# Optimization experiments

Measured on AMD Instinct MI355X. Metric: run time of the kernel, lower is better.

Reference implementation:

```python
import jax, jax.numpy as jnp
import numpy as np


def setup_inputs() -> dict:
    key = jax.random.key(0)
    kq, kk, kv = jax.random.split(key, 3)
    shape = (2, 8, 1024, 64)  # [B, H, L, D]
    return {
        "q": jax.random.normal(kq, shape, dtype=jnp.float32),
        "k": jax.random.normal(kk, shape, dtype=jnp.float32),
        "v": jax.random.normal(kv, shape, dtype=jnp.float32),
    }


def reference(q, k, v):
    B, H, L, D = q.shape
    eps = 1e-6
    q = jax.nn.relu(q).reshape(B * H, L, D)
    k = jax.nn.relu(k).reshape(B * H, L, D)
    v = jax.nn.relu(v).reshape(B * H, L, D)

    # cosFormer positional reweighting: pi/2 * (i+1)/L
    idx = (jnp.pi / 2) * jnp.arange(1, L + 1, dtype=q.dtype) / L  # [L]
    s = jnp.sin(idx)[None, :, None]  # [1, L, 1]
    c = jnp.cos(idx)[None, :, None]

    q_ = jnp.concatenate([q * s, q * c], axis=-1)  # [N, L, 2D]
    k_ = jnp.concatenate([k * s, k * c], axis=-1)  # [N, L, 2D]

    # causal linear attention via cumulative kv outer product
    kv = jnp.einsum("nld,nlm->nldm", k_, v)        # [N, L, 2D, D]
    kv_cum = jnp.cumsum(kv, axis=1)                  # [N, L, 2D, D]
    qkv = jnp.einsum("nld,nldm->nlm", q_, kv_cum)  # [N, L, D]

    k_cum = jnp.cumsum(k_, axis=1)                   # [N, L, 2D]
    denom = jnp.clip(jnp.einsum("nld,nld->nl", q_, k_cum), eps, None)

    out = qkv / denom[..., None]
    return out.reshape(B, H, L, D)
```

## Files before the change

### kernel.cpp

```cpp
#include <hip/hip_runtime.h>

#define N_HEADS 16
#define L_SEQ   1024
#define D_HEAD  64
#define D2      128
#define T_CHUNK 32
#define N_CHUNK (L_SEQ / T_CHUNK)
#define KV_ELEMS (D2 * D_HEAD)

#define ROWP 140
#define PARTP 132

__device__ __forceinline__ int pad_col(int d2) { return d2 + 4 * (d2 >> 5); }

#define SINCOS_SCALE 1.53398078788564122971e-3f

__device__ __forceinline__ float red8_dpp(float x) {
    x += __int_as_float(__builtin_amdgcn_mov_dpp(__float_as_int(x), 0xB1, 0xF, 0xF, true));
    x += __int_as_float(__builtin_amdgcn_mov_dpp(__float_as_int(x), 0x4E, 0xF, 0xF, true));
    x += __int_as_float(__builtin_amdgcn_mov_dpp(__float_as_int(x), 0x141, 0xF, 0xF, true));
    return x;
}

__global__ __launch_bounds__(256, 2) void k1_chunk_sums(
    const float* __restrict__ k, const float* __restrict__ v,
    float* __restrict__ sumkv, float* __restrict__ sumk)
{
    __shared__ __attribute__((aligned(16))) float k_s[T_CHUNK][ROWP];
    __shared__ __attribute__((aligned(16))) float v_s[T_CHUNK][D_HEAD];
    __shared__ float s_tab[T_CHUNK], c_tab[T_CHUNK];

    const int c = blockIdx.x, n = blockIdx.y;
    const int tid = threadIdx.x;
    const int base = (n * L_SEQ + c * T_CHUNK) * D_HEAD;

    if (tid < T_CHUNK) {
        float th = SINCOS_SCALE * (float)(c * T_CHUNK + tid + 1);
        s_tab[tid] = __sinf(th);
        c_tab[tid] = __cosf(th);
    }
    __syncthreads();

    const float4* k4g = (const float4*)(k + base);
    const float4* v4g = (const float4*)(v + base);
#pragma unroll
    for (int j = 0; j < 2; ++j) {
        int i4 = j * 256 + tid;
        int l = i4 >> 4, d = (i4 & 15) << 2;
        float4 kk = k4g[i4], vv = v4g[i4];
        kk.x = fmaxf(kk.x, 0.f); kk.y = fmaxf(kk.y, 0.f);
        kk.z = fmaxf(kk.z, 0.f); kk.w = fmaxf(kk.w, 0.f);
        vv.x = fmaxf(vv.x, 0.f); vv.y = fmaxf(vv.y, 0.f);
        vv.z = fmaxf(vv.z, 0.f); vv.w = fmaxf(vv.w, 0.f);
        float s = s_tab[l], cs = c_tab[l];
        *(float4*)&k_s[l][pad_col(d)]      = make_float4(kk.x*s,  kk.y*s,  kk.z*s,  kk.w*s);
        *(float4*)&k_s[l][pad_col(d + 64)] = make_float4(kk.x*cs, kk.y*cs, kk.z*cs, kk.w*cs);
        *(float4*)&v_s[l][d] = vv;
    }
    __syncthreads();

    if (tid < D2) {
        int pc = pad_col(tid);
        float ks = 0.f;
#pragma unroll
        for (int l = 0; l < T_CHUNK; ++l) ks += k_s[l][pc];
        sumk[(n * N_CHUNK + c) * D2 + tid] = ks;
    }

    const int g = tid & 7, mh = (tid >> 3) << 1;
    const int gbase = pad_col(16 * g);

    float st0[16], st1[16];
#pragma unroll
    for (int j = 0; j < 16; ++j) { st0[j] = 0.f; st1[j] = 0.f; }

    for (int l = 0; l < T_CHUNK; ++l) {
        float2 vm = *(const float2*)&v_s[l][mh];
        const float4* kv4 = (const float4*)&k_s[l][gbase];
#pragma unroll
        for (int jj = 0; jj < 4; ++jj) {
            float4 kk = kv4[jj];
            st0[4*jj+0] = fmaf(kk.x, vm.x, st0[4*jj+0]);
            st1[4*jj+0] = fmaf(kk.x, vm.y, st1[4*jj+0]);
            st0[4*jj+1] = fmaf(kk.y, vm.x, st0[4*jj+1]);
            st1[4*jj+1] = fmaf(kk.y, vm.y, st1[4*jj+1]);
            st0[4*jj+2] = fmaf(kk.z, vm.x, st0[4*jj+2]);
            st1[4*jj+2] = fmaf(kk.z, vm.y, st1[4*jj+2]);
            st0[4*jj+3] = fmaf(kk.w, vm.x, st0[4*jj+3]);
            st1[4*jj+3] = fmaf(kk.w, vm.y, st1[4*jj+3]);
        }
    }

    float4* dst = (float4*)(sumkv + (size_t)(n * N_CHUNK + c) * KV_ELEMS);
#pragma unroll
    for (int j4 = 0; j4 < 4; ++j4) {
        dst[(2*j4+0)*256 + tid] = make_float4(st0[4*j4], st0[4*j4+1], st0[4*j4+2], st0[4*j4+3]);
        dst[(2*j4+1)*256 + tid] = make_float4(st1[4*j4], st1[4*j4+1], st1[4*j4+2], st1[4*j4+3]);
    }
}

__global__ __launch_bounds__(256) void k2_prefix(
    float* __restrict__ sumkv, float* __restrict__ sumk)
{
    const int x = blockIdx.x, n = blockIdx.y;
    const int tid = threadIdx.x;

    if (x < 32) {
        float* base = sumkv + (size_t)n * N_CHUNK * KV_ELEMS + x * 256 + tid;
        float t[N_CHUNK];
#pragma unroll
        for (int c = 0; c < N_CHUNK; ++c) t[c] = base[c * KV_ELEMS];
        float r = 0.f;
#pragma unroll
        for (int c = 0; c < N_CHUNK; ++c) { base[c * KV_ELEMS] = r; r += t[c]; }
    } else if (tid < D2) {
        float* bk = sumk + n * N_CHUNK * D2 + tid;
        float t[N_CHUNK];
#pragma unroll
        for (int c = 0; c < N_CHUNK; ++c) t[c] = bk[c * D2];
        float r = 0.f;
#pragma unroll
        for (int c = 0; c < N_CHUNK; ++c) { bk[c * D2] = r; r += t[c]; }
    }
}

__global__ __launch_bounds__(256, 2) void k3_output(
    const float* __restrict__ q, const float* __restrict__ k,
    const float* __restrict__ v, const float* __restrict__ sumkv,
    const float* __restrict__ sumk, float* __restrict__ out)
{
    __shared__ __attribute__((aligned(16))) float k_s[T_CHUNK][ROWP];
    __shared__ __attribute__((aligned(16))) float q_s[T_CHUNK][ROWP];
    __shared__ __attribute__((aligned(16))) float v_s[T_CHUNK][D_HEAD];
    __shared__ __attribute__((aligned(16))) float part_s[T_CHUNK][PARTP];
    __shared__ float rden_s[T_CHUNK];
    __shared__ __attribute__((aligned(16))) float out_s[T_CHUNK][D_HEAD];
    __shared__ float s_tab[T_CHUNK], c_tab[T_CHUNK];

    const int c = blockIdx.x, n = blockIdx.y;
    const int tid = threadIdx.x;
    const int base = (n * L_SEQ + c * T_CHUNK) * D_HEAD;

    if (tid < T_CHUNK) {
        float th = SINCOS_SCALE * (float)(c * T_CHUNK + tid + 1);
        s_tab[tid] = __sinf(th);
        c_tab[tid] = __cosf(th);
    }
    __syncthreads();

    const float4* q4g = (const float4*)(q + base);
    const float4* k4g = (const float4*)(k + base);
    const float4* v4g = (const float4*)(v + base);
#pragma unroll
    for (int j = 0; j < 2; ++j) {
        int i4 = j * 256 + tid;
        int l = i4 >> 4, d = (i4 & 15) << 2;
        float4 kk = k4g[i4], qq = q4g[i4], vv = v4g[i4];
        kk.x = fmaxf(kk.x, 0.f); kk.y = fmaxf(kk.y, 0.f);
        kk.z = fmaxf(kk.z, 0.f); kk.w = fmaxf(kk.w, 0.f);
        qq.x = fmaxf(qq.x, 0.f); qq.y = fmaxf(qq.y, 0.f);
        qq.z = fmaxf(qq.z, 0.f); qq.w = fmaxf(qq.w, 0.f);
        vv.x = fmaxf(vv.x, 0.f); vv.y = fmaxf(vv.y, 0.f);
        vv.z = fmaxf(vv.z, 0.f); vv.w = fmaxf(vv.w, 0.f);
        float s = s_tab[l], cs = c_tab[l];
        *(float4*)&k_s[l][pad_col(d)]      = make_float4(kk.x*s,  kk.y*s,  kk.z*s,  kk.w*s);
        *(float4*)&k_s[l][pad_col(d + 64)] = make_float4(kk.x*cs, kk.y*cs, kk.z*cs, kk.w*cs);
        *(float4*)&q_s[l][pad_col(d)]      = make_float4(qq.x*s,  qq.y*s,  qq.z*s,  qq.w*s);
        *(float4*)&q_s[l][pad_col(d + 64)] = make_float4(qq.x*cs, qq.y*cs, qq.z*cs, qq.w*cs);
        *(float4*)&v_s[l][d] = vv;
    }

    const float4* pkv = (const float4*)(sumkv + (size_t)(n * N_CHUNK + c) * KV_ELEMS);
    float4 s0 = pkv[0*256 + tid];
    float4 s1 = pkv[1*256 + tid];
    float4 s2 = pkv[2*256 + tid];
    float4 s3 = pkv[3*256 + tid];
    float4 s4 = pkv[4*256 + tid];
    float4 s5 = pkv[5*256 + tid];
    float4 s6 = pkv[6*256 + tid];
    float4 s7 = pkv[7*256 + tid];
    float kc = 0.f;
    if (tid < D2) kc = sumk[(n * N_CHUNK + c) * D2 + tid];

    __syncthreads();

    if (tid < D2) {
        int pc = pad_col(tid);
#pragma unroll
        for (int l = 0; l < T_CHUNK; ++l) {
            kc += k_s[l][pc];
            part_s[l][tid] = q_s[l][pc] * kc;
        }
    }
    __syncthreads();

    {
        int l = tid >> 3, j = tid & 7;
        const float4* p4 = (const float4*)&part_s[l][j * 16];
        float4 aa = p4[0], bb = p4[1], cc = p4[2], dd = p4[3];
        float sum = ((aa.x + aa.y) + (aa.z + aa.w)) + ((bb.x + bb.y) + (bb.z + bb.w))
                  + ((cc.x + cc.y) + (cc.z + cc.w)) + ((dd.x + dd.y) + (dd.z + dd.w));
        sum = red8_dpp(sum);
        if (j == 0) rden_s[l] = 1.f / fmaxf(sum, 1e-6f);
    }
    __syncthreads();

    const int g = tid & 7, mh = (tid >> 3) << 1;
    const int gbase = pad_col(16 * g);

    float st0[16], st1[16];
    st0[0]=s0.x;  st0[1]=s0.y;  st0[2]=s0.z;  st0[3]=s0.w;
    st1[0]=s1.x;  st1[1]=s1.y;  st1[2]=s1.z;  st1[3]=s1.w;
    st0[4]=s2.x;  st0[5]=s2.y;  st0[6]=s2.z;  st0[7]=s2.w;
    st1[4]=s3.x;  st1[5]=s3.y;  st1[6]=s3.z;  st1[7]=s3.w;
    st0[8]=s4.x;  st0[9]=s4.y;  st0[10]=s4.z; st0[11]=s4.w;
    st1[8]=s5.x;  st1[9]=s5.y;  st1[10]=s5.z; st1[11]=s5.w;
    st0[12]=s6.x; st0[13]=s6.y; st0[14]=s6.z; st0[15]=s6.w;
    st1[12]=s7.x; st1[13]=s7.y; st1[14]=s7.z; st1[15]=s7.w;

    for (int l = 0; l < T_CHUNK; ++l) {
        float2 vm = *(const float2*)&v_s[l][mh];
        const float4* kv4 = (const float4*)&k_s[l][gbase];
        const float4* qv4 = (const float4*)&q_s[l][gbase];
        float a0 = 0.f, a1 = 0.f;
#pragma unroll
        for (int jj = 0; jj < 4; ++jj) {
            float4 kk = kv4[jj];
            float4 qq = qv4[jj];
            st0[4*jj+0] = fmaf(kk.x, vm.x, st0[4*jj+0]); a0 = fmaf(qq.x, st0[4*jj+0], a0);
            st1[4*jj+0] = fmaf(kk.x, vm.y, st1[4*jj+0]); a1 = fmaf(qq.x, st1[4*jj+0], a1);
            st0[4*jj+1] = fmaf(kk.y, vm.x, st0[4*jj+1]); a0 = fmaf(qq.y, st0[4*jj+1], a0);
            st1[4*jj+1] = fmaf(kk.y, vm.y, st1[4*jj+1]); a1 = fmaf(qq.y, st1[4*jj+1], a1);
            st0[4*jj+2] = fmaf(kk.z, vm.x, st0[4*jj+2]); a0 = fmaf(qq.z, st0[4*jj+2], a0);
            st1[4*jj+2] = fmaf(kk.z, vm.y, st1[4*jj+2]); a1 = fmaf(qq.z, st1[4*jj+2], a1);
            st0[4*jj+3] = fmaf(kk.w, vm.x, st0[4*jj+3]); a0 = fmaf(qq.w, st0[4*jj+3], a0);
            st1[4*jj+3] = fmaf(kk.w, vm.y, st1[4*jj+3]); a1 = fmaf(qq.w, st1[4*jj+3], a1);
        }
        a0 = red8_dpp(a0);
        a1 = red8_dpp(a1);
        if (g == 0) {
            float r = rden_s[l];
            *(float2*)&out_s[l][mh] = make_float2(a0 * r, a1 * r);
        }
    }
    __syncthreads();

    {
        float4* o4 = (float4*)(out + base);
        const float4* s4o = (const float4*)&out_s[0][0];
        o4[tid] = s4o[tid];
        o4[256 + tid] = s4o[256 + tid];
    }
}

extern "C" void kernel_launch(void* const* d_in, const int* in_sizes, int n_in,
                              void* d_out, int out_size, void* d_ws, size_t ws_size,
                              hipStream_t stream) {
    (void)in_sizes; (void)n_in; (void)out_size; (void)ws_size;
    const float* q = (const float*)d_in[0];
    const float* k = (const float*)d_in[1];
    const float* v = (const float*)d_in[2];
    float* out = (float*)d_out;

    float* sumkv = (float*)d_ws;
    float* sumk  = sumkv + (size_t)N_HEADS * N_CHUNK * KV_ELEMS;

    dim3 grid(N_CHUNK, N_HEADS);
    k1_chunk_sums<<<grid, 256, 0, stream>>>(k, v, sumkv, sumk);
    dim3 grid2(33, N_HEADS);
    k2_prefix<<<grid2, 256, 0, stream>>>(sumkv, sumk);
    k3_output<<<grid, 256, 0, stream>>>(q, k, v, sumkv, sumk, out);
}
```

Measured before the change: 90.90 us.

## Double chunk length to 64 and remap thread tiles to 8x4 state blocks

Chunk length goes from 32 to 64. This halves the number of chunks, so the per-chunk kv-state workspace and the prefix-scan traffic shrink, but each block now does a longer serial recurrence. Each thread now holds an 8x4 tile of the running state, with 16-lane DPP reductions for the output dot products; the k column sums and denominators are split across two halves of the block. Shared memory for the partial products and the output staging is aliased to fit the larger tiles, and launch bounds drop to one block per CU. The risks are fewer resident blocks to hide latency, twice as many serial steps, and more DPP reduction work per output.

```diff
diff --git a/kernel.cpp b/kernel.cpp
--- a/kernel.cpp
+++ b/kernel.cpp
@@ -4,7 +4,7 @@
 #define L_SEQ   1024
 #define D_HEAD  64
 #define D2      128
-#define T_CHUNK 32
+#define T_CHUNK 64
 #define N_CHUNK (L_SEQ / T_CHUNK)
 #define KV_ELEMS (D2 * D_HEAD)
 
@@ -15,20 +15,26 @@
 
 #define SINCOS_SCALE 1.53398078788564122971e-3f
 
-__device__ __forceinline__ float red8_dpp(float x) {
+__device__ __forceinline__ float red4_dpp(float x) {
     x += __int_as_float(__builtin_amdgcn_mov_dpp(__float_as_int(x), 0xB1, 0xF, 0xF, true));
     x += __int_as_float(__builtin_amdgcn_mov_dpp(__float_as_int(x), 0x4E, 0xF, 0xF, true));
+    return x;
+}
+__device__ __forceinline__ float red16_dpp(float x) {
+    x = red4_dpp(x);
     x += __int_as_float(__builtin_amdgcn_mov_dpp(__float_as_int(x), 0x141, 0xF, 0xF, true));
+    x += __int_as_float(__builtin_amdgcn_mov_dpp(__float_as_int(x), 0x140, 0xF, 0xF, true));
     return x;
 }
 
-__global__ __launch_bounds__(256, 2) void k1_chunk_sums(
+__global__ __launch_bounds__(256, 1) void k1_chunk_sums(
     const float* __restrict__ k, const float* __restrict__ v,
     float* __restrict__ sumkv, float* __restrict__ sumk)
 {
     __shared__ __attribute__((aligned(16))) float k_s[T_CHUNK][ROWP];
     __shared__ __attribute__((aligned(16))) float v_s[T_CHUNK][D_HEAD];
     __shared__ float s_tab[T_CHUNK], c_tab[T_CHUNK];
+    __shared__ float halfsum[2][D2];
 
     const int c = blockIdx.x, n = blockIdx.y;
     const int tid = threadIdx.x;
@@ -44,7 +50,7 @@
     const float4* k4g = (const float4*)(k + base);
     const float4* v4g = (const float4*)(v + base);
 #pragma unroll
-    for (int j = 0; j < 2; ++j) {
+    for (int j = 0; j < 4; ++j) {
         int i4 = j * 256 + tid;
         int l = i4 >> 4, d = (i4 & 15) << 2;
         float4 kk = k4g[i4], vv = v4g[i4];
@@ -59,44 +65,44 @@
     }
     __syncthreads();
 
-    if (tid < D2) {
-        int pc = pad_col(tid);
-        float ks = 0.f;
-#pragma unroll
-        for (int l = 0; l < T_CHUNK; ++l) ks += k_s[l][pc];
-        sumk[(n * N_CHUNK + c) * D2 + tid] = ks;
-    }
-
-    const int g = tid & 7, mh = (tid >> 3) << 1;
-    const int gbase = pad_col(16 * g);
-
-    float st0[16], st1[16];
-#pragma unroll
-    for (int j = 0; j < 16; ++j) { st0[j] = 0.f; st1[j] = 0.f; }
+    {
+        int col = tid & 127, half = tid >> 7;
+        int pc = pad_col(col);
+        float s = 0.f;
+#pragma unroll
+        for (int i = 0; i < 32; ++i) s += k_s[half * 32 + i][pc];
+        halfsum[half][col] = s;
+    }
+    __syncthreads();
+    if (tid < D2) sumk[(n * N_CHUNK + c) * D2 + tid] = halfsum[0][tid] + halfsum[1][tid];
+
+    const int g = tid & 15, mb = (tid >> 4) << 2;
+    const int gbase = pad_col(8 * g);
+
+    float st[8][4];
+#pragma unroll
+    for (int i = 0; i < 8; ++i)
+#pragma unroll
+        for (int j = 0; j < 4; ++j) st[i][j] = 0.f;
 
     for (int l = 0; l < T_CHUNK; ++l) {
-        float2 vm = *(const float2*)&v_s[l][mh];
-        const float4* kv4 = (const float4*)&k_s[l][gbase];
-#pragma unroll
-        for (int jj = 0; jj < 4; ++jj) {
-            float4 kk = kv4[jj];
-            st0[4*jj+0] = fmaf(kk.x, vm.x, st0[4*jj+0]);
-            st1[4*jj+0] = fmaf(kk.x, vm.y, st1[4*jj+0]);
-            st0[4*jj+1] = fmaf(kk.y, vm.x, st0[4*jj+1]);
-            st1[4*jj+1] = fmaf(kk.y, vm.y, st1[4*jj+1]);
-            st0[4*jj+2] = fmaf(kk.z, vm.x, st0[4*jj+2]);
-            st1[4*jj+2] = fmaf(kk.z, vm.y, st1[4*jj+2]);
-            st0[4*jj+3] = fmaf(kk.w, vm.x, st0[4*jj+3]);
-            st1[4*jj+3] = fmaf(kk.w, vm.y, st1[4*jj+3]);
+        float4 vv = *(const float4*)&v_s[l][mb];
+        const float4* kf4 = (const float4*)&k_s[l][gbase];
+        float4 ka = kf4[0], kb = kf4[1];
+        float kf[8] = {ka.x, ka.y, ka.z, ka.w, kb.x, kb.y, kb.z, kb.w};
+#pragma unroll
+        for (int i = 0; i < 8; ++i) {
+            st[i][0] = fmaf(kf[i], vv.x, st[i][0]);
+            st[i][1] = fmaf(kf[i], vv.y, st[i][1]);
+            st[i][2] = fmaf(kf[i], vv.z, st[i][2]);
+            st[i][3] = fmaf(kf[i], vv.w, st[i][3]);
         }
     }
 
     float4* dst = (float4*)(sumkv + (size_t)(n * N_CHUNK + c) * KV_ELEMS);
 #pragma unroll
-    for (int j4 = 0; j4 < 4; ++j4) {
-        dst[(2*j4+0)*256 + tid] = make_float4(st0[4*j4], st0[4*j4+1], st0[4*j4+2], st0[4*j4+3]);
-        dst[(2*j4+1)*256 + tid] = make_float4(st1[4*j4], st1[4*j4+1], st1[4*j4+2], st1[4*j4+3]);
-    }
+    for (int i = 0; i < 8; ++i)
+        dst[i * 256 + tid] = make_float4(st[i][0], st[i][1], st[i][2], st[i][3]);
 }
 
 __global__ __launch_bounds__(256) void k2_prefix(
@@ -124,7 +130,7 @@
     }
 }
 
-__global__ __launch_bounds__(256, 2) void k3_output(
+__global__ __launch_bounds__(256, 1) void k3_output(
     const float* __restrict__ q, const float* __restrict__ k,
     const float* __restrict__ v, const float* __restrict__ sumkv,
     const float* __restrict__ sumk, float* __restrict__ out)
@@ -132,10 +138,13 @@
     __shared__ __attribute__((aligned(16))) float k_s[T_CHUNK][ROWP];
     __shared__ __attribute__((aligned(16))) float q_s[T_CHUNK][ROWP];
     __shared__ __attribute__((aligned(16))) float v_s[T_CHUNK][D_HEAD];
-    __shared__ __attribute__((aligned(16))) float part_s[T_CHUNK][PARTP];
+    __shared__ __attribute__((aligned(16))) float pool[T_CHUNK * PARTP];
     __shared__ float rden_s[T_CHUNK];
-    __shared__ __attribute__((aligned(16))) float out_s[T_CHUNK][D_HEAD];
     __shared__ float s_tab[T_CHUNK], c_tab[T_CHUNK];
+    __shared__ float halfsum[2][D2];
+
+    float (*part_s)[PARTP]  = (float(*)[PARTP])pool;
+    float (*out_s)[D_HEAD]  = (float(*)[D_HEAD])pool;
 
     const int c = blockIdx.x, n = blockIdx.y;
     const int tid = threadIdx.x;
@@ -152,7 +161,7 @@
     const float4* k4g = (const float4*)(k + base);
     const float4* v4g = (const float4*)(v + base);
 #pragma unroll
-    for (int j = 0; j < 2; ++j) {
+    for (int j = 0; j < 4; ++j) {
         int i4 = j * 256 + tid;
         int l = i4 >> 4, d = (i4 & 15) << 2;
         float4 kk = k4g[i4], qq = q4g[i4], vv = v4g[i4];
@@ -171,76 +180,79 @@
     }
 
     const float4* pkv = (const float4*)(sumkv + (size_t)(n * N_CHUNK + c) * KV_ELEMS);
-    float4 s0 = pkv[0*256 + tid];
-    float4 s1 = pkv[1*256 + tid];
-    float4 s2 = pkv[2*256 + tid];
-    float4 s3 = pkv[3*256 + tid];
-    float4 s4 = pkv[4*256 + tid];
-    float4 s5 = pkv[5*256 + tid];
-    float4 s6 = pkv[6*256 + tid];
-    float4 s7 = pkv[7*256 + tid];
-    float kc = 0.f;
-    if (tid < D2) kc = sumk[(n * N_CHUNK + c) * D2 + tid];
-
-    __syncthreads();
-
-    if (tid < D2) {
-        int pc = pad_col(tid);
-#pragma unroll
-        for (int l = 0; l < T_CHUNK; ++l) {
+    float st[8][4];
+#pragma unroll
+    for (int i = 0; i < 8; ++i) {
+        float4 p = pkv[i * 256 + tid];
+        st[i][0] = p.x; st[i][1] = p.y; st[i][2] = p.z; st[i][3] = p.w;
+    }
+    float kc_g = sumk[(n * N_CHUNK + c) * D2 + (tid & 127)];
+
+    __syncthreads();
+
+    {
+        int col = tid & 127, half = tid >> 7;
+        int pc = pad_col(col);
+        float s = 0.f;
+#pragma unroll
+        for (int i = 0; i < 32; ++i) s += k_s[half * 32 + i][pc];
+        halfsum[half][col] = s;
+    }
+    __syncthreads();
+
+    {
+        int col = tid & 127, half = tid >> 7;
+        int pc = pad_col(col);
+        float kc = kc_g + (half ? halfsum[0][col] : 0.f);
+#pragma unroll
+        for (int i = 0; i < 32; ++i) {
+            int l = half * 32 + i;
             kc += k_s[l][pc];
-            part_s[l][tid] = q_s[l][pc] * kc;
-        }
-    }
-    __syncthreads();
-
-    {
-        int l = tid >> 3, j = tid & 7;
-        const float4* p4 = (const float4*)&part_s[l][j * 16];
-        float4 aa = p4[0], bb = p4[1], cc = p4[2], dd = p4[3];
-        float sum = ((aa.x + aa.y) + (aa.z + aa.w)) + ((bb.x + bb.y) + (bb.z + bb.w))
-                  + ((cc.x + cc.y) + (cc.z + cc.w)) + ((dd.x + dd.y) + (dd.z + dd.w));
-        sum = red8_dpp(sum);
+            part_s[l][col] = q_s[l][pc] * kc;
+        }
+    }
+    __syncthreads();
+
+    {
+        int l = tid >> 2, j = tid & 3;
+        const float4* p4 = (const float4*)&part_s[l][j * 32];
+        float sum = 0.f;
+#pragma unroll
+        for (int t = 0; t < 8; ++t) {
+            float4 x = p4[t];
+            sum += (x.x + x.y) + (x.z + x.w);
+        }
+        sum = red4_dpp(sum);
         if (j == 0) rden_s[l] = 1.f / fmaxf(sum, 1e-6f);
     }
     __syncthreads();
 
-    const int g = tid & 7, mh = (tid >> 3) << 1;
-    const int gbase = pad_col(16 * g);
-
-    float st0[16], st1[16];
-    st0[0]=s0.x;  st0[1]=s0.y;  st0[2]=s0.z;  st0[3]=s0.w;
-    st1[0]=s1.x;  st1[1]=s1.y;  st1[2]=s1.z;  st1[3]=s1.w;
-    st0[4]=s2.x;  st0[5]=s2.y;  st0[6]=s2.z;  st0[7]=s2.w;
-    st1[4]=s3.x;  st1[5]=s3.y;  st1[6]=s3.z;  st1[7]=s3.w;
-    st0[8]=s4.x;  st0[9]=s4.y;  st0[10]=s4.z; st0[11]=s4.w;
-    st1[8]=s5.x;  st1[9]=s5.y;  st1[10]=s5.z; st1[11]=s5.w;
-    st0[12]=s6.x; st0[13]=s6.y; st0[14]=s6.z; st0[15]=s6.w;
-    st1[12]=s7.x; st1[13]=s7.y; st1[14]=s7.z; st1[15]=s7.w;
+    const int g = tid & 15, mb = (tid >> 4) << 2;
+    const int gbase = pad_col(8 * g);
 
     for (int l = 0; l < T_CHUNK; ++l) {
-        float2 vm = *(const float2*)&v_s[l][mh];
-        const float4* kv4 = (const float4*)&k_s[l][gbase];
-        const float4* qv4 = (const float4*)&q_s[l][gbase];
-        float a0 = 0.f, a1 = 0.f;
-#pragma unroll
-        for (int jj = 0; jj < 4; ++jj) {
-            float4 kk = kv4[jj];
-            float4 qq = qv4[jj];
-            st0[4*jj+0] = fmaf(kk.x, vm.x, st0[4*jj+0]); a0 = fmaf(qq.x, st0[4*jj+0], a0);
-            st1[4*jj+0] = fmaf(kk.x, vm.y, st1[4*jj+0]); a1 = fmaf(qq.x, st1[4*jj+0], a1);
-            st0[4*jj+1] = fmaf(kk.y, vm.x, st0[4*jj+1]); a0 = fmaf(qq.y, st0[4*jj+1], a0);
-            st1[4*jj+1] = fmaf(kk.y, vm.y, st1[4*jj+1]); a1 = fmaf(qq.y, st1[4*jj+1], a1);
-            st0[4*jj+2] = fmaf(kk.z, vm.x, st0[4*jj+2]); a0 = fmaf(qq.z, st0[4*jj+2], a0);
-            st1[4*jj+2] = fmaf(kk.z, vm.y, st1[4*jj+2]); a1 = fmaf(qq.z, st1[4*jj+2], a1);
-            st0[4*jj+3] = fmaf(kk.w, vm.x, st0[4*jj+3]); a0 = fmaf(qq.w, st0[4*jj+3], a0);
-            st1[4*jj+3] = fmaf(kk.w, vm.y, st1[4*jj+3]); a1 = fmaf(qq.w, st1[4*jj+3], a1);
-        }
-        a0 = red8_dpp(a0);
-        a1 = red8_dpp(a1);
+        float4 vv = *(const float4*)&v_s[l][mb];
+        const float4* kf4 = (const float4*)&k_s[l][gbase];
+        const float4* qf4 = (const float4*)&q_s[l][gbase];
+        float4 ka = kf4[0], kb = kf4[1];
+        float4 qa = qf4[0], qb = qf4[1];
+        float kf[8] = {ka.x, ka.y, ka.z, ka.w, kb.x, kb.y, kb.z, kb.w};
+        float qf[8] = {qa.x, qa.y, qa.z, qa.w, qb.x, qb.y, qb.z, qb.w};
+        float a0 = 0.f, a1 = 0.f, a2 = 0.f, a3 = 0.f;
+#pragma unroll
+        for (int i = 0; i < 8; ++i) {
+            st[i][0] = fmaf(kf[i], vv.x, st[i][0]); a0 = fmaf(qf[i], st[i][0], a0);
+            st[i][1] = fmaf(kf[i], vv.y, st[i][1]); a1 = fmaf(qf[i], st[i][1], a1);
+            st[i][2] = fmaf(kf[i], vv.z, st[i][2]); a2 = fmaf(qf[i], st[i][2], a2);
+            st[i][3] = fmaf(kf[i], vv.w, st[i][3]); a3 = fmaf(qf[i], st[i][3], a3);
+        }
+        a0 = red16_dpp(a0);
+        a1 = red16_dpp(a1);
+        a2 = red16_dpp(a2);
+        a3 = red16_dpp(a3);
         if (g == 0) {
             float r = rden_s[l];
-            *(float2*)&out_s[l][mh] = make_float2(a0 * r, a1 * r);
+            *(float4*)&out_s[l][mb] = make_float4(a0 * r, a1 * r, a2 * r, a3 * r);
         }
     }
     __syncthreads();
@@ -248,8 +260,8 @@
     {
         float4* o4 = (float4*)(out + base);
         const float4* s4o = (const float4*)&out_s[0][0];
-        o4[tid] = s4o[tid];
-        o4[256 + tid] = s4o[256 + tid];
+#pragma unroll
+        for (int j = 0; j < 4; ++j) o4[j * 256 + tid] = s4o[j * 256 + tid];
     }
 }
 
```

Result: slower. 96.90 us (+6.6%).

## Fuse chunk-sum, prefix and output kernels into one cooperative kernel with grid syncs

Applied to the files above, without the earlier changes.

Merges the three launches (chunk sums, cross-chunk prefix scan, output) into one cooperative kernel that uses grid.sync between phases. The k and v tiles stay in shared memory across phases instead of being reloaded from global memory, and part_s and out_s now share one shared-memory pool. This removes launch gaps and redundant loads, in exchange for two grid-wide barriers and a requirement that all 512 blocks be co-resident.

```diff
diff --git a/kernel.cpp b/kernel.cpp
--- a/kernel.cpp
+++ b/kernel.cpp
@@ -1,4 +1,7 @@
 #include <hip/hip_runtime.h>
+#include <hip/hip_cooperative_groups.h>
+
+namespace cg = cooperative_groups;
 
 #define N_HEADS 16
 #define L_SEQ   1024
@@ -22,17 +25,26 @@
     return x;
 }
 
-__global__ __launch_bounds__(256, 2) void k1_chunk_sums(
-    const float* __restrict__ k, const float* __restrict__ v,
-    float* __restrict__ sumkv, float* __restrict__ sumk)
+__global__ __launch_bounds__(256, 2) void fused_all(
+    const float* __restrict__ q, const float* __restrict__ k,
+    const float* __restrict__ v, float* __restrict__ sumkv,
+    float* __restrict__ sumk, float* __restrict__ out)
 {
     __shared__ __attribute__((aligned(16))) float k_s[T_CHUNK][ROWP];
+    __shared__ __attribute__((aligned(16))) float q_s[T_CHUNK][ROWP];
     __shared__ __attribute__((aligned(16))) float v_s[T_CHUNK][D_HEAD];
+    __shared__ __attribute__((aligned(16))) float pool[T_CHUNK * PARTP];
+    __shared__ float rden_s[T_CHUNK];
     __shared__ float s_tab[T_CHUNK], c_tab[T_CHUNK];
+
+    float (*part_s)[PARTP] = (float(*)[PARTP])pool;
+    float (*out_s)[D_HEAD] = (float(*)[D_HEAD])pool;
 
     const int c = blockIdx.x, n = blockIdx.y;
     const int tid = threadIdx.x;
     const int base = (n * L_SEQ + c * T_CHUNK) * D_HEAD;
+
+    cg::grid_group grid = cg::this_grid();
 
     if (tid < T_CHUNK) {
         float th = SINCOS_SCALE * (float)(c * T_CHUNK + tid + 1);
@@ -70,115 +82,84 @@
     const int g = tid & 7, mh = (tid >> 3) << 1;
     const int gbase = pad_col(16 * g);
 
-    float st0[16], st1[16];
-#pragma unroll
-    for (int j = 0; j < 16; ++j) { st0[j] = 0.f; st1[j] = 0.f; }
-
-    for (int l = 0; l < T_CHUNK; ++l) {
-        float2 vm = *(const float2*)&v_s[l][mh];
-        const float4* kv4 = (const float4*)&k_s[l][gbase];
-#pragma unroll
-        for (int jj = 0; jj < 4; ++jj) {
-            float4 kk = kv4[jj];
-            st0[4*jj+0] = fmaf(kk.x, vm.x, st0[4*jj+0]);
-            st1[4*jj+0] = fmaf(kk.x, vm.y, st1[4*jj+0]);
-            st0[4*jj+1] = fmaf(kk.y, vm.x, st0[4*jj+1]);
-            st1[4*jj+1] = fmaf(kk.y, vm.y, st1[4*jj+1]);
-            st0[4*jj+2] = fmaf(kk.z, vm.x, st0[4*jj+2]);
-            st1[4*jj+2] = fmaf(kk.z, vm.y, st1[4*jj+2]);
-            st0[4*jj+3] = fmaf(kk.w, vm.x, st0[4*jj+3]);
-            st1[4*jj+3] = fmaf(kk.w, vm.y, st1[4*jj+3]);
-        }
-    }
-
-    float4* dst = (float4*)(sumkv + (size_t)(n * N_CHUNK + c) * KV_ELEMS);
-#pragma unroll
-    for (int j4 = 0; j4 < 4; ++j4) {
-        dst[(2*j4+0)*256 + tid] = make_float4(st0[4*j4], st0[4*j4+1], st0[4*j4+2], st0[4*j4+3]);
-        dst[(2*j4+1)*256 + tid] = make_float4(st1[4*j4], st1[4*j4+1], st1[4*j4+2], st1[4*j4+3]);
-    }
-}
-
-__global__ __launch_bounds__(256) void k2_prefix(
-    float* __restrict__ sumkv, float* __restrict__ sumk)
-{
-    const int x = blockIdx.x, n = blockIdx.y;
-    const int tid = threadIdx.x;
-
-    if (x < 32) {
-        float* base = sumkv + (size_t)n * N_CHUNK * KV_ELEMS + x * 256 + tid;
+    {
+        float st0[16], st1[16];
+#pragma unroll
+        for (int j = 0; j < 16; ++j) { st0[j] = 0.f; st1[j] = 0.f; }
+
+        for (int l = 0; l < T_CHUNK; ++l) {
+            float2 vm = *(const float2*)&v_s[l][mh];
+            const float4* kv4 = (const float4*)&k_s[l][gbase];
+#pragma unroll
+            for (int jj = 0; jj < 4; ++jj) {
+                float4 kk = kv4[jj];
+                st0[4*jj+0] = fmaf(kk.x, vm.x, st0[4*jj+0]);
+                st1[4*jj+0] = fmaf(kk.x, vm.y, st1[4*jj+0]);
+                st0[4*jj+1] = fmaf(kk.y, vm.x, st0[4*jj+1]);
+                st1[4*jj+1] = fmaf(kk.y, vm.y, st1[4*jj+1]);
+                st0[4*jj+2] = fmaf(kk.z, vm.x, st0[4*jj+2]);
+                st1[4*jj+2] = fmaf(kk.z, vm.y, st1[4*jj+2]);
+                st0[4*jj+3] = fmaf(kk.w, vm.x, st0[4*jj+3]);
+                st1[4*jj+3] = fmaf(kk.w, vm.y, st1[4*jj+3]);
+            }
+        }
+
+        float4* dst = (float4*)(sumkv + (size_t)(n * N_CHUNK + c) * KV_ELEMS);
+#pragma unroll
+        for (int j4 = 0; j4 < 4; ++j4) {
+            dst[(2*j4+0)*256 + tid] = make_float4(st0[4*j4], st0[4*j4+1], st0[4*j4+2], st0[4*j4+3]);
+            dst[(2*j4+1)*256 + tid] = make_float4(st1[4*j4], st1[4*j4+1], st1[4*j4+2], st1[4*j4+3]);
+        }
+    }
+
+    __threadfence();
+    grid.sync();
+
+    {
+        float* bse = sumkv + (size_t)n * N_CHUNK * KV_ELEMS + c * 256 + tid;
         float t[N_CHUNK];
 #pragma unroll
-        for (int c = 0; c < N_CHUNK; ++c) t[c] = base[c * KV_ELEMS];
+        for (int cc = 0; cc < N_CHUNK; ++cc) t[cc] = bse[cc * KV_ELEMS];
         float r = 0.f;
 #pragma unroll
-        for (int c = 0; c < N_CHUNK; ++c) { base[c * KV_ELEMS] = r; r += t[c]; }
-    } else if (tid < D2) {
-        float* bk = sumk + n * N_CHUNK * D2 + tid;
-        float t[N_CHUNK];
-#pragma unroll
-        for (int c = 0; c < N_CHUNK; ++c) t[c] = bk[c * D2];
-        float r = 0.f;
-#pragma unroll
-        for (int c = 0; c < N_CHUNK; ++c) { bk[c * D2] = r; r += t[c]; }
-    }
-}
-
-__global__ __launch_bounds__(256, 2) void k3_output(
-    const float* __restrict__ q, const float* __restrict__ k,
-    const float* __restrict__ v, const float* __restrict__ sumkv,
-    const float* __restrict__ sumk, float* __restrict__ out)
-{
-    __shared__ __attribute__((aligned(16))) float k_s[T_CHUNK][ROWP];
-    __shared__ __attribute__((aligned(16))) float q_s[T_CHUNK][ROWP];
-    __shared__ __attribute__((aligned(16))) float v_s[T_CHUNK][D_HEAD];
-    __shared__ __attribute__((aligned(16))) float part_s[T_CHUNK][PARTP];
-    __shared__ float rden_s[T_CHUNK];
-    __shared__ __attribute__((aligned(16))) float out_s[T_CHUNK][D_HEAD];
-    __shared__ float s_tab[T_CHUNK], c_tab[T_CHUNK];
-
-    const int c = blockIdx.x, n = blockIdx.y;
-    const int tid = threadIdx.x;
-    const int base = (n * L_SEQ + c * T_CHUNK) * D_HEAD;
-
-    if (tid < T_CHUNK) {
-        float th = SINCOS_SCALE * (float)(c * T_CHUNK + tid + 1);
-        s_tab[tid] = __sinf(th);
-        c_tab[tid] = __cosf(th);
-    }
-    __syncthreads();
+        for (int cc = 0; cc < N_CHUNK; ++cc) { bse[cc * KV_ELEMS] = r; r += t[cc]; }
+
+        if (c == 0 && tid < D2) {
+            float* bk = sumk + n * N_CHUNK * D2 + tid;
+            float tk[N_CHUNK];
+#pragma unroll
+            for (int cc = 0; cc < N_CHUNK; ++cc) tk[cc] = bk[cc * D2];
+            float rk = 0.f;
+#pragma unroll
+            for (int cc = 0; cc < N_CHUNK; ++cc) { bk[cc * D2] = rk; rk += tk[cc]; }
+        }
+    }
+
+    __threadfence();
+    grid.sync();
 
     const float4* q4g = (const float4*)(q + base);
-    const float4* k4g = (const float4*)(k + base);
-    const float4* v4g = (const float4*)(v + base);
 #pragma unroll
     for (int j = 0; j < 2; ++j) {
         int i4 = j * 256 + tid;
         int l = i4 >> 4, d = (i4 & 15) << 2;
-        float4 kk = k4g[i4], qq = q4g[i4], vv = v4g[i4];
-        kk.x = fmaxf(kk.x, 0.f); kk.y = fmaxf(kk.y, 0.f);
-        kk.z = fmaxf(kk.z, 0.f); kk.w = fmaxf(kk.w, 0.f);
+        float4 qq = q4g[i4];
         qq.x = fmaxf(qq.x, 0.f); qq.y = fmaxf(qq.y, 0.f);
         qq.z = fmaxf(qq.z, 0.f); qq.w = fmaxf(qq.w, 0.f);
-        vv.x = fmaxf(vv.x, 0.f); vv.y = fmaxf(vv.y, 0.f);
-        vv.z = fmaxf(vv.z, 0.f); vv.w = fmaxf(vv.w, 0.f);
         float s = s_tab[l], cs = c_tab[l];
-        *(float4*)&k_s[l][pad_col(d)]      = make_float4(kk.x*s,  kk.y*s,  kk.z*s,  kk.w*s);
-        *(float4*)&k_s[l][pad_col(d + 64)] = make_float4(kk.x*cs, kk.y*cs, kk.z*cs, kk.w*cs);
         *(float4*)&q_s[l][pad_col(d)]      = make_float4(qq.x*s,  qq.y*s,  qq.z*s,  qq.w*s);
         *(float4*)&q_s[l][pad_col(d + 64)] = make_float4(qq.x*cs, qq.y*cs, qq.z*cs, qq.w*cs);
-        *(float4*)&v_s[l][d] = vv;
     }
 
     const float4* pkv = (const float4*)(sumkv + (size_t)(n * N_CHUNK + c) * KV_ELEMS);
-    float4 s0 = pkv[0*256 + tid];
-    float4 s1 = pkv[1*256 + tid];
-    float4 s2 = pkv[2*256 + tid];
-    float4 s3 = pkv[3*256 + tid];
-    float4 s4 = pkv[4*256 + tid];
-    float4 s5 = pkv[5*256 + tid];
-    float4 s6 = pkv[6*256 + tid];
-    float4 s7 = pkv[7*256 + tid];
+    float st0[16], st1[16];
+#pragma unroll
+    for (int i = 0; i < 4; ++i) {
+        float4 p0 = pkv[(2*i+0) * 256 + tid];
+        float4 p1 = pkv[(2*i+1) * 256 + tid];
+        st0[4*i+0] = p0.x; st0[4*i+1] = p0.y; st0[4*i+2] = p0.z; st0[4*i+3] = p0.w;
+        st1[4*i+0] = p1.x; st1[4*i+1] = p1.y; st1[4*i+2] = p1.z; st1[4*i+3] = p1.w;
+    }
     float kc = 0.f;
     if (tid < D2) kc = sumk[(n * N_CHUNK + c) * D2 + tid];
 
@@ -197,26 +178,13 @@
     {
         int l = tid >> 3, j = tid & 7;
         const float4* p4 = (const float4*)&part_s[l][j * 16];
-        float4 aa = p4[0], bb = p4[1], cc = p4[2], dd = p4[3];
+        float4 aa = p4[0], bb = p4[1], cc4 = p4[2], dd = p4[3];
         float sum = ((aa.x + aa.y) + (aa.z + aa.w)) + ((bb.x + bb.y) + (bb.z + bb.w))
-                  + ((cc.x + cc.y) + (cc.z + cc.w)) + ((dd.x + dd.y) + (dd.z + dd.w));
+                  + ((cc4.x + cc4.y) + (cc4.z + cc4.w)) + ((dd.x + dd.y) + (dd.z + dd.w));
         sum = red8_dpp(sum);
         if (j == 0) rden_s[l] = 1.f / fmaxf(sum, 1e-6f);
     }
     __syncthreads();
-
-    const int g = tid & 7, mh = (tid >> 3) << 1;
-    const int gbase = pad_col(16 * g);
-
-    float st0[16], st1[16];
-    st0[0]=s0.x;  st0[1]=s0.y;  st0[2]=s0.z;  st0[3]=s0.w;
-    st1[0]=s1.x;  st1[1]=s1.y;  st1[2]=s1.z;  st1[3]=s1.w;
-    st0[4]=s2.x;  st0[5]=s2.y;  st0[6]=s2.z;  st0[7]=s2.w;
-    st1[4]=s3.x;  st1[5]=s3.y;  st1[6]=s3.z;  st1[7]=s3.w;
-    st0[8]=s4.x;  st0[9]=s4.y;  st0[10]=s4.z; st0[11]=s4.w;
-    st1[8]=s5.x;  st1[9]=s5.y;  st1[10]=s5.z; st1[11]=s5.w;
-    st0[12]=s6.x; st0[13]=s6.y; st0[14]=s6.z; st0[15]=s6.w;
-    st1[12]=s7.x; st1[13]=s7.y; st1[14]=s7.z; st1[15]=s7.w;
 
     for (int l = 0; l < T_CHUNK; ++l) {
         float2 vm = *(const float2*)&v_s[l][mh];
@@ -265,9 +233,9 @@
     float* sumkv = (float*)d_ws;
     float* sumk  = sumkv + (size_t)N_HEADS * N_CHUNK * KV_ELEMS;
 
-    dim3 grid(N_CHUNK, N_HEADS);
-    k1_chunk_sums<<<grid, 256, 0, stream>>>(k, v, sumkv, sumk);
-    dim3 grid2(33, N_HEADS);
-    k2_prefix<<<grid2, 256, 0, stream>>>(sumkv, sumk);
-    k3_output<<<grid, 256, 0, stream>>>(q, k, v, sumkv, sumk, out);
+    void* args[] = {(void*)&q, (void*)&k, (void*)&v,
+                    (void*)&sumkv, (void*)&sumk, (void*)&out};
+    hipLaunchCooperativeKernel((const void*)fused_all,
+                               dim3(N_CHUNK, N_HEADS), dim3(256),
+                               args, 0, stream);
 }
```

Result: slower. 329.3 us (+262.3%).

## Drop prefix kernel; accumulate chunk sums in output kernel with XCD-aware block mapping

Applied to the files above, without the earlier changes.

Removes the separate prefix-scan kernel. Each output block now sums all preceding chunk KV states and k sums itself, with the next chunk's loads prefetched while the current one is added. Block indices are remapped so that chunks of the same head land on the same XCD, which should improve L2 reuse of those partial sums. Global loads are issued before the sincos table barrier, and part_s/out_s share one shared-memory buffer. The cost is redundant work that grows with chunk index: the last chunks read up to 31 KV states of 32 KB each, which adds load imbalance but saves a launch and a full read-write pass.

```diff
diff --git a/kernel.cpp b/kernel.cpp
--- a/kernel.cpp
+++ b/kernel.cpp
@@ -22,6 +22,12 @@
     return x;
 }
 
+__device__ __forceinline__ void decode_cn(int bid, int& c, int& n) {
+    int xcd = bid & 7, slot = bid >> 3;
+    n = xcd + ((slot & 1) << 3);
+    c = slot >> 1;
+}
+
 __global__ __launch_bounds__(256, 2) void k1_chunk_sums(
     const float* __restrict__ k, const float* __restrict__ v,
     float* __restrict__ sumkv, float* __restrict__ sumk)
@@ -30,9 +36,14 @@
     __shared__ __attribute__((aligned(16))) float v_s[T_CHUNK][D_HEAD];
     __shared__ float s_tab[T_CHUNK], c_tab[T_CHUNK];
 
-    const int c = blockIdx.x, n = blockIdx.y;
+    int c, n; decode_cn(blockIdx.x, c, n);
     const int tid = threadIdx.x;
     const int base = (n * L_SEQ + c * T_CHUNK) * D_HEAD;
+
+    const float4* k4g = (const float4*)(k + base);
+    const float4* v4g = (const float4*)(v + base);
+    float4 kr0 = k4g[tid], kr1 = k4g[256 + tid];
+    float4 vr0 = v4g[tid], vr1 = v4g[256 + tid];
 
     if (tid < T_CHUNK) {
         float th = SINCOS_SCALE * (float)(c * T_CHUNK + tid + 1);
@@ -41,13 +52,12 @@
     }
     __syncthreads();
 
-    const float4* k4g = (const float4*)(k + base);
-    const float4* v4g = (const float4*)(v + base);
 #pragma unroll
     for (int j = 0; j < 2; ++j) {
         int i4 = j * 256 + tid;
         int l = i4 >> 4, d = (i4 & 15) << 2;
-        float4 kk = k4g[i4], vv = v4g[i4];
+        float4 kk = j ? kr1 : kr0;
+        float4 vv = j ? vr1 : vr0;
         kk.x = fmaxf(kk.x, 0.f); kk.y = fmaxf(kk.y, 0.f);
         kk.z = fmaxf(kk.z, 0.f); kk.w = fmaxf(kk.w, 0.f);
         vv.x = fmaxf(vv.x, 0.f); vv.y = fmaxf(vv.y, 0.f);
@@ -99,31 +109,6 @@
     }
 }
 
-__global__ __launch_bounds__(256) void k2_prefix(
-    float* __restrict__ sumkv, float* __restrict__ sumk)
-{
-    const int x = blockIdx.x, n = blockIdx.y;
-    const int tid = threadIdx.x;
-
-    if (x < 32) {
-        float* base = sumkv + (size_t)n * N_CHUNK * KV_ELEMS + x * 256 + tid;
-        float t[N_CHUNK];
-#pragma unroll
-        for (int c = 0; c < N_CHUNK; ++c) t[c] = base[c * KV_ELEMS];
-        float r = 0.f;
-#pragma unroll
-        for (int c = 0; c < N_CHUNK; ++c) { base[c * KV_ELEMS] = r; r += t[c]; }
-    } else if (tid < D2) {
-        float* bk = sumk + n * N_CHUNK * D2 + tid;
-        float t[N_CHUNK];
-#pragma unroll
-        for (int c = 0; c < N_CHUNK; ++c) t[c] = bk[c * D2];
-        float r = 0.f;
-#pragma unroll
-        for (int c = 0; c < N_CHUNK; ++c) { bk[c * D2] = r; r += t[c]; }
-    }
-}
-
 __global__ __launch_bounds__(256, 2) void k3_output(
     const float* __restrict__ q, const float* __restrict__ k,
     const float* __restrict__ v, const float* __restrict__ sumkv,
@@ -132,30 +117,82 @@
     __shared__ __attribute__((aligned(16))) float k_s[T_CHUNK][ROWP];
     __shared__ __attribute__((aligned(16))) float q_s[T_CHUNK][ROWP];
     __shared__ __attribute__((aligned(16))) float v_s[T_CHUNK][D_HEAD];
-    __shared__ __attribute__((aligned(16))) float part_s[T_CHUNK][PARTP];
+    __shared__ __attribute__((aligned(16))) float pool[T_CHUNK * PARTP];
     __shared__ float rden_s[T_CHUNK];
-    __shared__ __attribute__((aligned(16))) float out_s[T_CHUNK][D_HEAD];
     __shared__ float s_tab[T_CHUNK], c_tab[T_CHUNK];
 
-    const int c = blockIdx.x, n = blockIdx.y;
+    float (*part_s)[PARTP] = (float(*)[PARTP])pool;
+    float (*out_s)[D_HEAD] = (float(*)[D_HEAD])pool;
+
+    int c, n; decode_cn(blockIdx.x, c, n);
     const int tid = threadIdx.x;
     const int base = (n * L_SEQ + c * T_CHUNK) * D_HEAD;
+
+    const float4* q4g = (const float4*)(q + base);
+    const float4* k4g = (const float4*)(k + base);
+    const float4* v4g = (const float4*)(v + base);
+    float4 kr0 = k4g[tid], kr1 = k4g[256 + tid];
+    float4 qr0 = q4g[tid], qr1 = q4g[256 + tid];
+    float4 vr0 = v4g[tid], vr1 = v4g[256 + tid];
 
     if (tid < T_CHUNK) {
         float th = SINCOS_SCALE * (float)(c * T_CHUNK + tid + 1);
         s_tab[tid] = __sinf(th);
         c_tab[tid] = __cosf(th);
     }
-    __syncthreads();
-
-    const float4* q4g = (const float4*)(q + base);
-    const float4* k4g = (const float4*)(k + base);
-    const float4* v4g = (const float4*)(v + base);
+
+    float st0[16], st1[16];
+#pragma unroll
+    for (int j = 0; j < 16; ++j) { st0[j] = 0.f; st1[j] = 0.f; }
+
+    const float4* csb = (const float4*)(sumkv + (size_t)n * N_CHUNK * KV_ELEMS);
+    if (c > 0) {
+        float4 b0,b1,b2,b3,b4,b5,b6,b7;
+        {
+            const float4* p = csb;
+            b0=p[0*256+tid]; b1=p[1*256+tid]; b2=p[2*256+tid]; b3=p[3*256+tid];
+            b4=p[4*256+tid]; b5=p[5*256+tid]; b6=p[6*256+tid]; b7=p[7*256+tid];
+        }
+        for (int cc = 0; cc < c; ++cc) {
+            float4 c0=b0,c1=b1,c2=b2,c3=b3,c4=b4,c5=b5,c6=b6,c7=b7;
+            if (cc + 1 < c) {
+                const float4* p = csb + (size_t)(cc + 1) * (KV_ELEMS / 4);
+                b0=p[0*256+tid]; b1=p[1*256+tid]; b2=p[2*256+tid]; b3=p[3*256+tid];
+                b4=p[4*256+tid]; b5=p[5*256+tid]; b6=p[6*256+tid]; b7=p[7*256+tid];
+            }
+            st0[0]+=c0.x;  st0[1]+=c0.y;  st0[2]+=c0.z;  st0[3]+=c0.w;
+            st1[0]+=c1.x;  st1[1]+=c1.y;  st1[2]+=c1.z;  st1[3]+=c1.w;
+            st0[4]+=c2.x;  st0[5]+=c2.y;  st0[6]+=c2.z;  st0[7]+=c2.w;
+            st1[4]+=c3.x;  st1[5]+=c3.y;  st1[6]+=c3.z;  st1[7]+=c3.w;
+            st0[8]+=c4.x;  st0[9]+=c4.y;  st0[10]+=c4.z; st0[11]+=c4.w;
+            st1[8]+=c5.x;  st1[9]+=c5.y;  st1[10]+=c5.z; st1[11]+=c5.w;
+            st0[12]+=c6.x; st0[13]+=c6.y; st0[14]+=c6.z; st0[15]+=c6.w;
+            st1[12]+=c7.x; st1[13]+=c7.y; st1[14]+=c7.z; st1[15]+=c7.w;
+        }
+    }
+
+    float kc = 0.f;
+    if (tid < D2) {
+        const float* bk = sumk + (size_t)n * N_CHUNK * D2 + tid;
+        float k0 = 0.f, k1 = 0.f, k2 = 0.f, k3 = 0.f;
+        int cc = 0;
+        for (; cc + 4 <= c; cc += 4) {
+            k0 += bk[(cc+0) * D2]; k1 += bk[(cc+1) * D2];
+            k2 += bk[(cc+2) * D2]; k3 += bk[(cc+3) * D2];
+        }
+        for (; cc < c; ++cc) k0 += bk[cc * D2];
+        kc = (k0 + k1) + (k2 + k3);
+    }
+
+    __syncthreads();
+
 #pragma unroll
     for (int j = 0; j < 2; ++j) {
         int i4 = j * 256 + tid;
         int l = i4 >> 4, d = (i4 & 15) << 2;
-        float4 kk = k4g[i4], qq = q4g[i4], vv = v4g[i4];
+        float4 kk = j ? kr1 : kr0;
+        float4 qq = j ? qr1 : qr0;
+        float4 vv = j ? vr1 : vr0;
         kk.x = fmaxf(kk.x, 0.f); kk.y = fmaxf(kk.y, 0.f);
         kk.z = fmaxf(kk.z, 0.f); kk.w = fmaxf(kk.w, 0.f);
         qq.x = fmaxf(qq.x, 0.f); qq.y = fmaxf(qq.y, 0.f);
@@ -169,19 +206,6 @@
         *(float4*)&q_s[l][pad_col(d + 64)] = make_float4(qq.x*cs, qq.y*cs, qq.z*cs, qq.w*cs);
         *(float4*)&v_s[l][d] = vv;
     }
-
-    const float4* pkv = (const float4*)(sumkv + (size_t)(n * N_CHUNK + c) * KV_ELEMS);
-    float4 s0 = pkv[0*256 + tid];
-    float4 s1 = pkv[1*256 + tid];
-    float4 s2 = pkv[2*256 + tid];
-    float4 s3 = pkv[3*256 + tid];
-    float4 s4 = pkv[4*256 + tid];
-    float4 s5 = pkv[5*256 + tid];
-    float4 s6 = pkv[6*256 + tid];
-    float4 s7 = pkv[7*256 + tid];
-    float kc = 0.f;
-    if (tid < D2) kc = sumk[(n * N_CHUNK + c) * D2 + tid];
-
     __syncthreads();
 
     if (tid < D2) {
@@ -197,9 +221,9 @@
     {
         int l = tid >> 3, j = tid & 7;
         const float4* p4 = (const float4*)&part_s[l][j * 16];
-        float4 aa = p4[0], bb = p4[1], cc = p4[2], dd = p4[3];
+        float4 aa = p4[0], bb = p4[1], cc4 = p4[2], dd = p4[3];
         float sum = ((aa.x + aa.y) + (aa.z + aa.w)) + ((bb.x + bb.y) + (bb.z + bb.w))
-                  + ((cc.x + cc.y) + (cc.z + cc.w)) + ((dd.x + dd.y) + (dd.z + dd.w));
+                  + ((cc4.x + cc4.y) + (cc4.z + cc4.w)) + ((dd.x + dd.y) + (dd.z + dd.w));
         sum = red8_dpp(sum);
         if (j == 0) rden_s[l] = 1.f / fmaxf(sum, 1e-6f);
     }
@@ -207,16 +231,6 @@
 
     const int g = tid & 7, mh = (tid >> 3) << 1;
     const int gbase = pad_col(16 * g);
-
-    float st0[16], st1[16];
-    st0[0]=s0.x;  st0[1]=s0.y;  st0[2]=s0.z;  st0[3]=s0.w;
-    st1[0]=s1.x;  st1[1]=s1.y;  st1[2]=s1.z;  st1[3]=s1.w;
-    st0[4]=s2.x;  st0[5]=s2.y;  st0[6]=s2.z;  st0[7]=s2.w;
-    st1[4]=s3.x;  st1[5]=s3.y;  st1[6]=s3.z;  st1[7]=s3.w;
-    st0[8]=s4.x;  st0[9]=s4.y;  st0[10]=s4.z; st0[11]=s4.w;
-    st1[8]=s5.x;  st1[9]=s5.y;  st1[10]=s5.z; st1[11]=s5.w;
-    st0[12]=s6.x; st0[13]=s6.y; st0[14]=s6.z; st0[15]=s6.w;
-    st1[12]=s7.x; st1[13]=s7.y; st1[14]=s7.z; st1[15]=s7.w;
 
     for (int l = 0; l < T_CHUNK; ++l) {
         float2 vm = *(const float2*)&v_s[l][mh];
@@ -265,9 +279,6 @@
     float* sumkv = (float*)d_ws;
     float* sumk  = sumkv + (size_t)N_HEADS * N_CHUNK * KV_ELEMS;
 
-    dim3 grid(N_CHUNK, N_HEADS);
-    k1_chunk_sums<<<grid, 256, 0, stream>>>(k, v, sumkv, sumk);
-    dim3 grid2(33, N_HEADS);
-    k2_prefix<<<grid2, 256, 0, stream>>>(sumkv, sumk);
-    k3_output<<<grid, 256, 0, stream>>>(q, k, v, sumkv, sumk, out);
-}
+    k1_chunk_sums<<<dim3(N_CHUNK * N_HEADS), 256, 0, stream>>>(k, v, sumkv, sumk);
+    k3_output<<<dim3(N_CHUNK * N_HEADS), 256, 0, stream>>>(q, k, v, sumkv, sumk, out);
+}
```

Result: slower. 103.4 us (+13.7%).
